# Performance work log

Hardware: AMD Instinct MI355X
Metric: run time of the kernel (lower is better)

Reference implementation:

```python
import jax, jax.numpy as jnp
import numpy as np
from jax import lax

ALPHA = -30.0  # softmin temperature from module init
EPS = 1e-4     # matches `+ 0.0001` in _softMinShapeletSeries


def _sliding_softmin(series, shp):
    """Sliding-window mean-squared distance between each shapelet and every
    window of each series, followed by softmin pooling over windows.
    series: [N, T], shp: [K, L] -> [N, K].
    Uses the identity mean((x_win - s)^2) = (sum(x_win^2) - 2<x_win, s> + sum(s^2)) / L
    so the sliding distances become two VALID cross-correlations.
    """
    N, T = series.shape
    K, L = shp.shape
    dn = lax.conv_dimension_numbers((N, 1, T), (K, 1, L), ('NCH', 'OIH', 'NCH'))
    # <x_win, s> for all windows/shapelets: [N, K, W], W = T - L + 1
    xdot = lax.conv_general_dilated(series[:, None, :], shp[:, None, :], (1,), 'VALID',
                                    dimension_numbers=dn)
    dn1 = lax.conv_dimension_numbers((N, 1, T), (1, 1, L), ('NCH', 'OIH', 'NCH'))
    # sum(x_win^2) via correlation with ones kernel: [N, 1, W]
    sumx2 = lax.conv_general_dilated((series * series)[:, None, :],
                                     jnp.ones((1, 1, L), series.dtype), (1,), 'VALID',
                                     dimension_numbers=dn1)
    s2 = jnp.sum(shp * shp, axis=1)  # [K]
    d = (sumx2 - 2.0 * xdot + s2[None, :, None]) / L  # [N, K, W]
    e = jnp.exp(ALPHA * d) + EPS
    return jnp.sum(d * e, axis=2) / jnp.sum(e, axis=2)  # [N, K]


def setup_inputs() -> dict:
    key = jax.random.key(0)
    ks = jax.random.split(key, 6)
    N, T = 512, 2048
    K = 64            # nb_shapelets
    Ls = (32, 64, 96) # shapelet lengths: s * shapelets_size, s = 1..scale
    n_classes = 10
    return {
        'series': jax.random.normal(ks[0], (N, T), jnp.float32),
        'shp1': jax.random.normal(ks[1], (K, Ls[0]), jnp.float32),
        'shp2': jax.random.normal(ks[2], (K, Ls[1]), jnp.float32),
        'shp3': jax.random.normal(ks[3], (K, Ls[2]), jnp.float32),
        'W': jax.random.normal(ks[4], (3 * K, n_classes), jnp.float32) * 0.05,
        'b': jax.random.normal(ks[5], (n_classes,), jnp.float32) * 0.05,
    }


def reference(series, shp1, shp2, shp3, W, b):
    # concat softmin features per scale, in shapelet order (matches torch.cat order)
    sm = jnp.concatenate([_sliding_softmin(series, s) for s in (shp1, shp2, shp3)], axis=1)
    logits = sm @ W + b  # nn.Linear
    return jax.nn.softmax(logits, axis=-1)  # output_size_ > 1 branch
```

## Files before the change

### kernel.cpp

```cpp
#include <hip/hip_runtime.h>
#include <hip/hip_bf16.h>

#define ALPHA_ (-30.0f)
#define EPS_ (1e-4f)
#define LOG2E_ (1.4426950408889634f)

typedef short bf16x8 __attribute__((ext_vector_type(8)));
typedef float f32x4 __attribute__((ext_vector_type(4)));
typedef float f32x2 __attribute__((ext_vector_type(2)));

__device__ __forceinline__ short f2bf(float f) {
  __hip_bfloat16 h = __float2bfloat16(f);
  return __builtin_bit_cast(short, h);
}

__device__ __forceinline__ bf16x8 ld_a(const short* p) {
  int2 lo = *reinterpret_cast<const int2*>(p);
  int2 hi = *reinterpret_cast<const int2*>(p + 4);
  union { int i[4]; bf16x8 v; } u;
  u.i[0] = lo.x; u.i[1] = lo.y; u.i[2] = hi.x; u.i[3] = hi.y;
  return u.v;
}

__device__ __forceinline__ bf16x8 ld_b(const short* p) {
  union { int4 i; bf16x8 v; } u;
  u.i = *reinterpret_cast<const int4*>(p);
  return u.v;
}

#define XC_OFF 0
#define PS_OFF 17536
#define R2_OFF 25744
#define S2_OFF 33936
#define RED_OFF 34064
#define SMEM_BYTES 36112
#define CL 2192

template <int L, int SCALE>
__device__ __forceinline__ void feat_impl(const float* __restrict__ series,
                                          const float* __restrict__ shp,
                                          float* __restrict__ F, char* smem,
                                          int sg0) {
  constexpr int T = 2048;
  constexpr int W = T - L + 1;
  constexpr int KT = L / 32;
  constexpr int M = W / 128;
  constexpr float CE = ALPHA_ * LOG2E_ / (float)L;
  constexpr float SCL = -2.0f * CE;

  short* xc = (short*)(smem + XC_OFF);
  float* ps = (float*)(smem + PS_OFF);
  short* sh = (short*)(smem + R2_OFF);
  float* sx = (float*)(smem + R2_OFF);
  float* s2 = (float*)(smem + S2_OFF);
  float* red = (float*)(smem + RED_OFF);

  const int n = blockIdx.x;
  const int tid = threadIdx.x;
  const int lane = tid & 63;
  const int wg = tid >> 6;
  const int col = lane & 15;
  const int kg = lane >> 4;

  const float* srow = series + (size_t)n * T;
  float4 v0 = *reinterpret_cast<const float4*>(srow + tid * 8);
  float4 v1 = *reinterpret_cast<const float4*>(srow + tid * 8 + 4);
  float xv[8] = {v0.x, v0.y, v0.z, v0.w, v1.x, v1.y, v1.z, v1.w};
  short bv8[12];
#pragma unroll
  for (int i = 0; i < 8; ++i) bv8[i] = f2bf(xv[i]);
  if (tid < 255) {
    float4 ve = *reinterpret_cast<const float4*>(srow + tid * 8 + 8);
    bv8[8] = f2bf(ve.x); bv8[9] = f2bf(ve.y);
    bv8[10] = f2bf(ve.z); bv8[11] = f2bf(ve.w);
  } else {
    bv8[8] = bv8[9] = bv8[10] = bv8[11] = 0;
  }

  float loc[8];
  float run = 0.f;
#pragma unroll
  for (int i = 0; i < 8; ++i) {
    run = fmaf(xv[i], xv[i], run);
    loc[i] = run;
  }
  float sc = run;
#pragma unroll
  for (int off = 1; off < 64; off <<= 1) {
    float t = __shfl_up(sc, off, 64);
    if (lane >= off) sc += t;
  }
  if (lane == 63) red[wg] = sc;
  __syncthreads();
  float wb0 = 0.f;
  for (int w = 0; w < wg; ++w) wb0 += red[w];
  float excl = wb0 + sc - run;
#pragma unroll
  for (int i = 0; i < 8; ++i) ps[tid * 8 + 1 + i] = excl + loc[i];
  if (tid == 0) ps[0] = 0.f;

#pragma unroll
  for (int c = 0; c < 4; ++c) {
    union { short s[8]; int4 q; } u;
#pragma unroll
    for (int i = 0; i < 8; ++i) u.s[i] = bv8[i + c];
    *reinterpret_cast<int4*>(xc + c * CL + tid * 8) = u.q;
  }
  if (tid < CL - 2048) {
    int j = 2048 + tid;
#pragma unroll
    for (int c = 0; c < 4; ++c) xc[c * CL + j] = 0;
  }

  const float* shB = shp + sg0 * 32 * L;
  {
    constexpr int NE = 32 * L;
    for (int i4 = tid * 4; i4 < NE; i4 += 1024) {
      float4 v = *reinterpret_cast<const float4*>(shB + i4);
      union { short s[4]; int2 q; } u;
      u.s[0] = f2bf(v.x * SCL); u.s[1] = f2bf(v.y * SCL);
      u.s[2] = f2bf(v.z * SCL); u.s[3] = f2bf(v.w * SCL);
      *reinterpret_cast<int2*>(sh + i4) = u.q;
    }
  }
  {
    constexpr int LQ = L / 8;
    const float* sp = shB + (tid & 31) * L + (tid >> 5) * LQ;
    float s = 0.f;
#pragma unroll
    for (int l = 0; l < LQ; ++l) s = fmaf(sp[l], sp[l], s);
    red[256 + tid] = s;
  }
  __syncthreads();
  if (tid < 32) {
    float s = 0.f;
#pragma unroll
    for (int p = 0; p < 8; ++p) s += red[256 + p * 32 + tid];
    s2[tid] = CE * s;
  }
  __syncthreads();

  bf16x8 bfr[KT][2];
#pragma unroll
  for (int kt = 0; kt < KT; ++kt)
#pragma unroll
    for (int j = 0; j < 2; ++j)
      bfr[kt][j] = ld_b(sh + (j * 16 + col) * L + kt * 32 + kg * 8);
  float s2c[2];
#pragma unroll
  for (int j = 0; j < 2; ++j) s2c[j] = s2[j * 16 + col];
  __syncthreads();

  for (int w = tid; w < 2048; w += 256)
    sx[w] = (w < W) ? CE * (ps[w + L] - ps[w]) : 0.f;
  __syncthreads();

  const int cc = lane & 3;
  const short* ap = xc + cc * CL + (col - cc) + 8 * kg + wg * 32;
  const float* sp2 = sx + wg * 32 + kg * 4;

  f32x2 esP[2], dsP[2];
#pragma unroll
  for (int j = 0; j < 2; ++j) {
    esP[j] = (f32x2){0.f, 0.f};
    dsP[j] = (f32x2){0.f, 0.f};
  }

  for (int it = 0; it < M; ++it) {
    f32x4 acc[2][2];
#pragma unroll
    for (int t = 0; t < 2; ++t)
#pragma unroll
      for (int j = 0; j < 2; ++j)
        acc[t][j] = (f32x4){s2c[j], s2c[j], s2c[j], s2c[j]};
#pragma unroll
    for (int kt = 0; kt < KT; ++kt) {
      bf16x8 a0 = ld_a(ap + kt * 32);
      bf16x8 a1 = ld_a(ap + 16 + kt * 32);
#pragma unroll
      for (int j = 0; j < 2; ++j) {
        acc[0][j] = __builtin_amdgcn_mfma_f32_16x16x32_bf16(a0, bfr[kt][j],
                                                            acc[0][j], 0, 0, 0);
        acc[1][j] = __builtin_amdgcn_mfma_f32_16x16x32_bf16(a1, bfr[kt][j],
                                                            acc[1][j], 0, 0, 0);
      }
    }
    float4 sv0 = *reinterpret_cast<const float4*>(sp2);
    float4 sv1 = *reinterpret_cast<const float4*>(sp2 + 16);
    f32x2 sxa[2][2] = {{{sv0.x, sv0.y}, {sv0.z, sv0.w}},
                       {{sv1.x, sv1.y}, {sv1.z, sv1.w}}};
#pragma unroll
    for (int t = 0; t < 2; ++t) {
#pragma unroll
      for (int j = 0; j < 2; ++j) {
        f32x2 u0 = (f32x2){acc[t][j][0], acc[t][j][1]} + sxa[t][0];
        f32x2 u1 = (f32x2){acc[t][j][2], acc[t][j][3]} + sxa[t][1];
        f32x2 e0, e1;
        e0.x = __builtin_amdgcn_exp2f(u0.x);
        e0.y = __builtin_amdgcn_exp2f(u0.y);
        e1.x = __builtin_amdgcn_exp2f(u1.x);
        e1.y = __builtin_amdgcn_exp2f(u1.y);
        e0 += (f32x2){EPS_, EPS_};
        e1 += (f32x2){EPS_, EPS_};
        esP[j] += e0;
        esP[j] += e1;
        dsP[j] = __builtin_elementwise_fma(u0, e0, dsP[j]);
        dsP[j] = __builtin_elementwise_fma(u1, e1, dsP[j]);
      }
    }
    ap += 128;
    sp2 += 128;
  }
  {
    f32x4 acc[2][2];
#pragma unroll
    for (int t = 0; t < 2; ++t)
#pragma unroll
      for (int j = 0; j < 2; ++j)
        acc[t][j] = (f32x4){s2c[j], s2c[j], s2c[j], s2c[j]};
#pragma unroll
    for (int kt = 0; kt < KT; ++kt) {
      bf16x8 a0 = ld_a(ap + kt * 32);
      bf16x8 a1 = ld_a(ap + 16 + kt * 32);
#pragma unroll
      for (int j = 0; j < 2; ++j) {
        acc[0][j] = __builtin_amdgcn_mfma_f32_16x16x32_bf16(a0, bfr[kt][j],
                                                            acc[0][j], 0, 0, 0);
        acc[1][j] = __builtin_amdgcn_mfma_f32_16x16x32_bf16(a1, bfr[kt][j],
                                                            acc[1][j], 0, 0, 0);
      }
    }
#pragma unroll
    for (int t = 0; t < 2; ++t) {
      const int wb = M * 128 + wg * 32 + t * 16 + kg * 4;
      float4 sv = *reinterpret_cast<const float4*>(sp2 + t * 16);
      const float svr[4] = {sv.x, sv.y, sv.z, sv.w};
#pragma unroll
      for (int j = 0; j < 2; ++j) {
#pragma unroll
        for (int r = 0; r < 4; ++r) {
          float u = acc[t][j][r] + svr[r];
          float e = __builtin_amdgcn_exp2f(u) + EPS_;
          float em = ((wb + r) < W) ? e : 0.f;
          esP[j].x += em;
          dsP[j].x = fmaf(u, em, dsP[j].x);
        }
      }
    }
  }

  constexpr float ALc = ALPHA_ * LOG2E_;
  float fe[2], fd[2];
#pragma unroll
  for (int j = 0; j < 2; ++j) {
    float es = esP[j].x + esP[j].y;
    float ds = dsP[j].x + dsP[j].y;
    es += __shfl_xor(es, 16, 64);
    es += __shfl_xor(es, 32, 64);
    ds += __shfl_xor(ds, 16, 64);
    ds += __shfl_xor(ds, 32, 64);
    fe[j] = es;
    fd[j] = ds;
  }
  __syncthreads();
  if (lane < 16) {
#pragma unroll
    for (int j = 0; j < 2; ++j) {
      int slot = (wg * 2 + j) * 16 + lane;
      red[slot] = fe[j];
      red[128 + slot] = fd[j];
    }
  }
  __syncthreads();
  if (tid < 32) {
    const int j = tid >> 4, c = tid & 15;
    float es = 0.f, ds = 0.f;
#pragma unroll
    for (int w = 0; w < 4; ++w) {
      int slot = (w * 2 + j) * 16 + c;
      es += red[slot];
      ds += red[128 + slot];
    }
    F[n * 192 + SCALE * 64 + sg0 * 32 + tid] = ds / (es * ALc);
  }
}

__global__ void __launch_bounds__(256, 2)
feat_kernel(const float* __restrict__ series, const float* __restrict__ shp1,
            const float* __restrict__ shp2, const float* __restrict__ shp3,
            float* __restrict__ F) {
  __shared__ __align__(16) char smem[SMEM_BYTES];
  const int sg0 = blockIdx.y & 1;
  const int scale = blockIdx.y >> 1;
  if (scale == 0)
    feat_impl<32, 0>(series, shp1, F, smem, sg0);
  else if (scale == 1)
    feat_impl<64, 1>(series, shp2, F, smem, sg0);
  else
    feat_impl<96, 2>(series, shp3, F, smem, sg0);
}

__global__ void __launch_bounds__(64) logits_kernel(const float* __restrict__ F,
                                                    const float* __restrict__ Wm,
                                                    const float* __restrict__ bv,
                                                    float* __restrict__ out) {
  __shared__ float Ws[1920];
  __shared__ float bs[16];
  const int tid = threadIdx.x;
  for (int i = tid; i < 1920; i += 64) Ws[i] = Wm[i];
  if (tid < 10) bs[tid] = bv[tid];
  __syncthreads();

  const int n = blockIdx.x * 64 + tid;
  float acc[10];
#pragma unroll
  for (int c = 0; c < 10; ++c) acc[c] = bs[c];
  const float* f = F + n * 192;
  for (int j = 0; j < 192; j += 4) {
    float4 v = *reinterpret_cast<const float4*>(f + j);
#pragma unroll
    for (int c = 0; c < 10; ++c)
      acc[c] += v.x * Ws[(j + 0) * 10 + c] + v.y * Ws[(j + 1) * 10 + c] +
                v.z * Ws[(j + 2) * 10 + c] + v.w * Ws[(j + 3) * 10 + c];
  }
  float m = acc[0];
#pragma unroll
  for (int c = 1; c < 10; ++c) m = fmaxf(m, acc[c]);
  float s = 0.f;
  float e[10];
#pragma unroll
  for (int c = 0; c < 10; ++c) {
    e[c] = exp2f((acc[c] - m) * LOG2E_);
    s += e[c];
  }
  float inv = 1.f / s;
#pragma unroll
  for (int c = 0; c < 10; ++c) out[n * 10 + c] = e[c] * inv;
}

extern "C" void kernel_launch(void* const* d_in, const int* in_sizes, int n_in,
                              void* d_out, int out_size, void* d_ws, size_t ws_size,
                              hipStream_t stream) {
  const float* series = (const float*)d_in[0];
  const float* shp1 = (const float*)d_in[1];
  const float* shp2 = (const float*)d_in[2];
  const float* shp3 = (const float*)d_in[3];
  const float* Wm = (const float*)d_in[4];
  const float* bv = (const float*)d_in[5];
  float* out = (float*)d_out;
  float* F = (float*)d_ws;

  feat_kernel<<<dim3(512, 6), 256, 0, stream>>>(series, shp1, shp2, shp3, F);
  logits_kernel<<<8, 64, 0, stream>>>(F, Wm, bv, out);
}
```

Measured before the change: 58.77 us.

## Double-buffer LDS operand loads across iterations and shrink shared memory footprint

The main MFMA loop is software-pipelined: the A fragments and window-energy terms for the next iteration are loaded from LDS into a second register set while the current iteration computes. The sx term is folded into the accumulator initialisation instead of being added after the MFMAs. The LDS layout is compacted (smaller padded row length, sx aliased onto the prefix-sum buffer with a register staging step), which lowers shared memory per block and may allow more resident blocks. The cost is higher register pressure from the doubled fragment buffers, which could reduce occupancy.

```diff
diff --git a/kernel.cpp b/kernel.cpp
--- a/kernel.cpp
+++ b/kernel.cpp
@@ -29,12 +29,12 @@
 }
 
 #define XC_OFF 0
-#define PS_OFF 17536
-#define R2_OFF 25744
-#define S2_OFF 33936
-#define RED_OFF 34064
-#define SMEM_BYTES 36112
-#define CL 2192
+#define PS_OFF 17152
+#define SH_OFF 25360
+#define S2_OFF 31504
+#define RED_OFF 31632
+#define SMEM_BYTES 32656
+#define CL 2144
 
 template <int L, int SCALE>
 __device__ __forceinline__ void feat_impl(const float* __restrict__ series,
@@ -50,8 +50,8 @@
 
   short* xc = (short*)(smem + XC_OFF);
   float* ps = (float*)(smem + PS_OFF);
-  short* sh = (short*)(smem + R2_OFF);
-  float* sx = (float*)(smem + R2_OFF);
+  float* sx = (float*)(smem + PS_OFF);
+  short* sh = (short*)(smem + SH_OFF);
   float* s2 = (float*)(smem + S2_OFF);
   float* red = (float*)(smem + RED_OFF);
 
@@ -123,19 +123,22 @@
       *reinterpret_cast<int2*>(sh + i4) = u.q;
     }
   }
+  float s2p;
   {
     constexpr int LQ = L / 8;
     const float* sp = shB + (tid & 31) * L + (tid >> 5) * LQ;
     float s = 0.f;
 #pragma unroll
     for (int l = 0; l < LQ; ++l) s = fmaf(sp[l], sp[l], s);
-    red[256 + tid] = s;
-  }
+    s2p = s;
+  }
+  __syncthreads();
+  red[tid] = s2p;
   __syncthreads();
   if (tid < 32) {
     float s = 0.f;
 #pragma unroll
-    for (int p = 0; p < 8; ++p) s += red[256 + p * 32 + tid];
+    for (int p = 0; p < 8; ++p) s += red[p * 32 + tid];
     s2[tid] = CE * s;
   }
   __syncthreads();
@@ -149,15 +152,25 @@
   float s2c[2];
 #pragma unroll
   for (int j = 0; j < 2; ++j) s2c[j] = s2[j * 16 + col];
-  __syncthreads();
-
-  for (int w = tid; w < 2048; w += 256)
-    sx[w] = (w < W) ? CE * (ps[w + L] - ps[w]) : 0.f;
+
+  float pv[8], pvL[8];
+#pragma unroll
+  for (int i = 0; i < 8; ++i) {
+    int w = tid + i * 256;
+    pv[i] = ps[w];
+    pvL[i] = (w < W) ? ps[w + L] : 0.f;
+  }
+  __syncthreads();
+#pragma unroll
+  for (int i = 0; i < 8; ++i) {
+    int w = tid + i * 256;
+    sx[w] = (w < W) ? CE * (pvL[i] - pv[i]) : 0.f;
+  }
   __syncthreads();
 
   const int cc = lane & 3;
-  const short* ap = xc + cc * CL + (col - cc) + 8 * kg + wg * 32;
-  const float* sp2 = sx + wg * 32 + kg * 4;
+  const short* apb = xc + cc * CL + (col - cc) + 8 * kg + wg * 32;
+  const float* sxb = sx + wg * 32 + kg * 4;
 
   f32x2 esP[2], dsP[2];
 #pragma unroll
@@ -166,80 +179,93 @@
     dsP[j] = (f32x2){0.f, 0.f};
   }
 
-  for (int it = 0; it < M; ++it) {
+  bf16x8 aA[2 * KT], aB[2 * KT];
+  float4 svA0, svA1, svB0, svB1;
+
+#define LOADIT(AF, S0, S1, it)                                            \
+  do {                                                                    \
+    const short* _p = apb + (it) * 128;                                   \
+    _Pragma("unroll") for (int kt = 0; kt < KT; ++kt) {                   \
+      AF[kt] = ld_a(_p + kt * 32);                                        \
+      AF[KT + kt] = ld_a(_p + 16 + kt * 32);                              \
+    }                                                                     \
+    const float* _s = sxb + (it) * 128;                                   \
+    S0 = *reinterpret_cast<const float4*>(_s);                            \
+    S1 = *reinterpret_cast<const float4*>(_s + 16);                       \
+  } while (0)
+
+#define BODYIT(AF, S0, S1)                                                \
+  do {                                                                    \
+    f32x4 s40 = (f32x4){S0.x, S0.y, S0.z, S0.w};                          \
+    f32x4 s41 = (f32x4){S1.x, S1.y, S1.z, S1.w};                          \
+    f32x4 acc[2][2];                                                      \
+    _Pragma("unroll") for (int j = 0; j < 2; ++j) {                       \
+      acc[0][j] = s40 + s2c[j];                                           \
+      acc[1][j] = s41 + s2c[j];                                           \
+    }                                                                     \
+    _Pragma("unroll") for (int kt = 0; kt < KT; ++kt) {                   \
+      _Pragma("unroll") for (int j = 0; j < 2; ++j) {                     \
+        acc[0][j] = __builtin_amdgcn_mfma_f32_16x16x32_bf16(              \
+            AF[kt], bfr[kt][j], acc[0][j], 0, 0, 0);                      \
+        acc[1][j] = __builtin_amdgcn_mfma_f32_16x16x32_bf16(              \
+            AF[KT + kt], bfr[kt][j], acc[1][j], 0, 0, 0);                 \
+      }                                                                   \
+    }                                                                     \
+    _Pragma("unroll") for (int t = 0; t < 2; ++t) {                       \
+      _Pragma("unroll") for (int j = 0; j < 2; ++j) {                     \
+        f32x2 u0 = (f32x2){acc[t][j][0], acc[t][j][1]};                   \
+        f32x2 u1 = (f32x2){acc[t][j][2], acc[t][j][3]};                   \
+        f32x2 e0, e1;                                                     \
+        e0.x = __builtin_amdgcn_exp2f(u0.x);                              \
+        e0.y = __builtin_amdgcn_exp2f(u0.y);                              \
+        e1.x = __builtin_amdgcn_exp2f(u1.x);                              \
+        e1.y = __builtin_amdgcn_exp2f(u1.y);                              \
+        e0 += (f32x2){EPS_, EPS_};                                        \
+        e1 += (f32x2){EPS_, EPS_};                                        \
+        esP[j] += e0;                                                     \
+        esP[j] += e1;                                                     \
+        dsP[j] = __builtin_elementwise_fma(u0, e0, dsP[j]);               \
+        dsP[j] = __builtin_elementwise_fma(u1, e1, dsP[j]);               \
+      }                                                                   \
+    }                                                                     \
+  } while (0)
+
+  LOADIT(aA, svA0, svA1, 0);
+  for (int it = 0; it < M - 1; it += 2) {
+    LOADIT(aB, svB0, svB1, it + 1);
+    BODYIT(aA, svA0, svA1);
+    LOADIT(aA, svA0, svA1, it + 2);
+    BODYIT(aB, svB0, svB1);
+  }
+  LOADIT(aB, svB0, svB1, M);
+  BODYIT(aA, svA0, svA1);
+  {
+    f32x4 s40 = (f32x4){svB0.x, svB0.y, svB0.z, svB0.w};
+    f32x4 s41 = (f32x4){svB1.x, svB1.y, svB1.z, svB1.w};
     f32x4 acc[2][2];
 #pragma unroll
-    for (int t = 0; t < 2; ++t)
-#pragma unroll
-      for (int j = 0; j < 2; ++j)
-        acc[t][j] = (f32x4){s2c[j], s2c[j], s2c[j], s2c[j]};
+    for (int j = 0; j < 2; ++j) {
+      acc[0][j] = s40 + s2c[j];
+      acc[1][j] = s41 + s2c[j];
+    }
 #pragma unroll
     for (int kt = 0; kt < KT; ++kt) {
-      bf16x8 a0 = ld_a(ap + kt * 32);
-      bf16x8 a1 = ld_a(ap + 16 + kt * 32);
 #pragma unroll
       for (int j = 0; j < 2; ++j) {
-        acc[0][j] = __builtin_amdgcn_mfma_f32_16x16x32_bf16(a0, bfr[kt][j],
-                                                            acc[0][j], 0, 0, 0);
-        acc[1][j] = __builtin_amdgcn_mfma_f32_16x16x32_bf16(a1, bfr[kt][j],
-                                                            acc[1][j], 0, 0, 0);
-      }
-    }
-    float4 sv0 = *reinterpret_cast<const float4*>(sp2);
-    float4 sv1 = *reinterpret_cast<const float4*>(sp2 + 16);
-    f32x2 sxa[2][2] = {{{sv0.x, sv0.y}, {sv0.z, sv0.w}},
-                       {{sv1.x, sv1.y}, {sv1.z, sv1.w}}};
-#pragma unroll
-    for (int t = 0; t < 2; ++t) {
-#pragma unroll
-      for (int j = 0; j < 2; ++j) {
-        f32x2 u0 = (f32x2){acc[t][j][0], acc[t][j][1]} + sxa[t][0];
-        f32x2 u1 = (f32x2){acc[t][j][2], acc[t][j][3]} + sxa[t][1];
-        f32x2 e0, e1;
-        e0.x = __builtin_amdgcn_exp2f(u0.x);
-        e0.y = __builtin_amdgcn_exp2f(u0.y);
-        e1.x = __builtin_amdgcn_exp2f(u1.x);
-        e1.y = __builtin_amdgcn_exp2f(u1.y);
-        e0 += (f32x2){EPS_, EPS_};
-        e1 += (f32x2){EPS_, EPS_};
-        esP[j] += e0;
-        esP[j] += e1;
-        dsP[j] = __builtin_elementwise_fma(u0, e0, dsP[j]);
-        dsP[j] = __builtin_elementwise_fma(u1, e1, dsP[j]);
-      }
-    }
-    ap += 128;
-    sp2 += 128;
-  }
-  {
-    f32x4 acc[2][2];
-#pragma unroll
-    for (int t = 0; t < 2; ++t)
-#pragma unroll
-      for (int j = 0; j < 2; ++j)
-        acc[t][j] = (f32x4){s2c[j], s2c[j], s2c[j], s2c[j]};
-#pragma unroll
-    for (int kt = 0; kt < KT; ++kt) {
-      bf16x8 a0 = ld_a(ap + kt * 32);
-      bf16x8 a1 = ld_a(ap + 16 + kt * 32);
-#pragma unroll
-      for (int j = 0; j < 2; ++j) {
-        acc[0][j] = __builtin_amdgcn_mfma_f32_16x16x32_bf16(a0, bfr[kt][j],
-                                                            acc[0][j], 0, 0, 0);
-        acc[1][j] = __builtin_amdgcn_mfma_f32_16x16x32_bf16(a1, bfr[kt][j],
-                                                            acc[1][j], 0, 0, 0);
+        acc[0][j] = __builtin_amdgcn_mfma_f32_16x16x32_bf16(
+            aB[kt], bfr[kt][j], acc[0][j], 0, 0, 0);
+        acc[1][j] = __builtin_amdgcn_mfma_f32_16x16x32_bf16(
+            aB[KT + kt], bfr[kt][j], acc[1][j], 0, 0, 0);
       }
     }
 #pragma unroll
     for (int t = 0; t < 2; ++t) {
       const int wb = M * 128 + wg * 32 + t * 16 + kg * 4;
-      float4 sv = *reinterpret_cast<const float4*>(sp2 + t * 16);
-      const float svr[4] = {sv.x, sv.y, sv.z, sv.w};
 #pragma unroll
       for (int j = 0; j < 2; ++j) {
 #pragma unroll
         for (int r = 0; r < 4; ++r) {
-          float u = acc[t][j][r] + svr[r];
+          float u = acc[t][j][r];
           float e = __builtin_amdgcn_exp2f(u) + EPS_;
           float em = ((wb + r) < W) ? e : 0.f;
           esP[j].x += em;
@@ -248,6 +274,8 @@
       }
     }
   }
+#undef LOADIT
+#undef BODYIT
 
   constexpr float ALc = ALPHA_ * LOG2E_;
   float fe[2], fd[2];
```

After: 61.22 us. +4.2%, slower.
